# Performance work log

Measured on AMD Instinct MI355X. Metric: run time of the kernel, lower is better.

Reference implementation:

```python
import jax, jax.numpy as jnp
import numpy as np

B, S, D = 2, 2048, 1024
H, KVH, HD = 16, 1, 64
E, K, HID = 8, 2, 4096
EPS = 1e-5


def rmsnorm(x, scale):
    ms = jnp.mean(x * x, axis=-1, keepdims=True)
    return x * jax.lax.rsqrt(ms + EPS) * scale


def setup_inputs() -> dict:
    key = jax.random.key(0)
    ks = jax.random.split(key, 12)
    s = lambda k, shape, fan: jax.random.normal(k, shape, jnp.float32) * (fan ** -0.5)
    return {
        "x": jax.random.normal(ks[0], (B, S, D), jnp.float32),
        "g_pre_mqa": jnp.ones((D,), jnp.float32),
        "g_post_mqa": jnp.ones((D,), jnp.float32),
        "g_pre_moe": jnp.ones((D,), jnp.float32),
        "g_post_moe": jnp.ones((D,), jnp.float32),
        "Wq": s(ks[1], (D, H * HD), D),
        "Wk": s(ks[2], (D, KVH * HD), D),
        "Wv": s(ks[3], (D, KVH * HD), D),
        "Wo": s(ks[4], (H * HD, D), H * HD),
        "Wg": s(ks[5], (D, E), D),
        "We1": s(ks[6], (E, D, HID), D),
        "We2": s(ks[7], (E, HID, D), HID),
    }


def mqa(x, Wq, Wk, Wv, Wo):
    b, s, _ = x.shape
    q = (x @ Wq).reshape(b, s, H, HD).transpose(0, 2, 1, 3)     # [B,H,S,hd]
    k = (x @ Wk).reshape(b, s, KVH, HD).transpose(0, 2, 1, 3)   # [B,1,S,hd]
    v = (x @ Wv).reshape(b, s, KVH, HD).transpose(0, 2, 1, 3)
    scores = jnp.einsum('bhqd,bhkd->bhqk', q, jnp.broadcast_to(k, (b, H, s, HD))) / np.sqrt(HD)
    probs = jax.nn.softmax(scores, axis=-1)  # note: no causal mask, matching _standard_attention
    out = jnp.einsum('bhqk,bhkd->bhqd', probs, jnp.broadcast_to(v, (b, H, s, HD)))
    out = out.transpose(0, 2, 1, 3).reshape(b, s, H * HD)
    return out @ Wo


def moe(h, Wg, We1, We2):
    logits = h @ Wg                       # [B,S,E]
    probs = jax.nn.softmax(logits, axis=-1)
    topv, topi = jax.lax.top_k(probs, K)  # [B,S,K]
    # scatter top-k probs into full expert vector (non-chosen experts -> 0)
    routing = jnp.sum(jax.nn.one_hot(topi, E, dtype=h.dtype) * topv[..., None], axis=-2)  # [B,S,E]
    mid = jax.nn.gelu(jnp.einsum('bsd,edh->bseh', h, We1))
    eo = jnp.einsum('bseh,ehd->bsed', mid, We2)
    out = jnp.einsum('bse,bsed->bsd', routing, eo)
    return out, probs


def reference(x, g_pre_mqa, g_post_mqa, g_pre_moe, g_post_moe, Wq, Wk, Wv, Wo, Wg, We1, We2):
    # inference path: dropout and router noise disabled (training=False)
    x = x + rmsnorm(mqa(rmsnorm(x, g_pre_mqa), Wq, Wk, Wv, Wo), g_post_mqa)
    moe_out, routing_probs = moe(rmsnorm(x, g_pre_moe), Wg, We1, We2)
    x = x + rmsnorm(moe_out, g_post_moe)
    return x, routing_probs
```

## Files before the change

kernel.cpp:

```cpp
#include <hip/hip_runtime.h>
#include <hip/hip_bf16.h>
#include <math.h>

#define NTOK   4096
#define DMODEL 1024
#define SEQL   2048
#define QKVW   1152
#define NH     16
#define HDIM   64
#define NE     8
#define HIDD   4096
#define EPSV   1e-5f
#define KT     32

#define ASCL   256.f
#define WSCL   4096.f
#define OUTSCL (1.f/1048576.f)
#define SSCALE (0.125f/65536.f)
#define PBIAS  10.397207708399179f
#define DTHR   0.5f

typedef __attribute__((ext_vector_type(8))) short bf16x8;
typedef __attribute__((ext_vector_type(8))) _Float16 f16x8;
typedef __attribute__((ext_vector_type(4))) _Float16 f16x4;
typedef __attribute__((ext_vector_type(4))) float f32x4;

#define GLOBAL_AS __attribute__((address_space(1)))
#define LDS_AS    __attribute__((address_space(3)))
__device__ __forceinline__ void gl_lds16(const void* g, void* l){
  __builtin_amdgcn_global_load_lds((const GLOBAL_AS void*)g, (LDS_AS void*)l, 16u, 0, 0u);
}

__device__ __forceinline__ short f2b(float x){
  __hip_bfloat16 h = __float2bfloat16(x);
  return *reinterpret_cast<short*>(&h);
}
__device__ __forceinline__ void split2h(float x, _Float16& a, _Float16& b){
  a = (_Float16)x;
  b = (_Float16)(x - (float)a);
}

__global__ __launch_bounds__(256) void transpose_conv_kernel(
    const float* __restrict__ in, short* __restrict__ out,
    int R, int C, long inb, long outb)
{
  __shared__ float tile[32][33];
  in  += (size_t)blockIdx.z * inb;
  out += (size_t)blockIdx.z * outb;
  int c0 = blockIdx.x*32, r0 = blockIdx.y*32;
  int tx = threadIdx.x & 31, ty = threadIdx.x >> 5;
  #pragma unroll
  for (int i=0;i<4;i++)
    tile[ty+i*8][tx] = in[(size_t)(r0+ty+i*8)*C + c0+tx];
  __syncthreads();
  int cl = threadIdx.x >> 3, quad = threadIdx.x & 7;
  short4 s;
  s.x = f2b(tile[quad*4+0][cl]);
  s.y = f2b(tile[quad*4+1][cl]);
  s.z = f2b(tile[quad*4+2][cl]);
  s.w = f2b(tile[quad*4+3][cl]);
  *(short4*)&out[(size_t)(c0+cl)*R + r0 + quad*4] = s;
}

__global__ __launch_bounds__(256) void transpose_split2f16_kernel(
    const float* __restrict__ in, _Float16* __restrict__ o1, _Float16* __restrict__ o2,
    int R, int C, int rowOff, int outLD)
{
  __shared__ float tile[32][33];
  int c0 = blockIdx.x*32, r0 = blockIdx.y*32;
  int tx = threadIdx.x & 31, ty = threadIdx.x >> 5;
  #pragma unroll
  for (int i=0;i<4;i++)
    tile[ty+i*8][tx] = in[(size_t)(r0+ty+i*8)*C + c0+tx];
  __syncthreads();
  #pragma unroll
  for (int i=0;i<4;i++){
    float v = tile[tx][ty+i*8] * WSCL;
    _Float16 va,vb; split2h(v,va,vb);
    size_t idx = (size_t)(c0+ty+i*8+rowOff)*outLD + r0+tx;
    o1[idx]=va; o2[idx]=vb;
  }
}

__global__ __launch_bounds__(256) void rms_split2_kernel(
    const float* __restrict__ x, const float* __restrict__ g,
    _Float16* __restrict__ o1, _Float16* __restrict__ o2)
{
  int row = blockIdx.x, tid = threadIdx.x;
  const float4* xr = (const float4*)(x + (size_t)row*DMODEL);
  float4 v = xr[tid];
  float ss = v.x*v.x + v.y*v.y + v.z*v.z + v.w*v.w;
  #pragma unroll
  for (int off=32; off; off>>=1) ss += __shfl_down(ss, off);
  __shared__ float red[4];
  if ((tid&63)==0) red[tid>>6] = ss;
  __syncthreads();
  float rs = rsqrtf((red[0]+red[1]+red[2]+red[3])*(1.f/1024.f) + EPSV) * ASCL;
  float4 gv = ((const float4*)g)[tid];
  float o[4] = {v.x*rs*gv.x, v.y*rs*gv.y, v.z*rs*gv.z, v.w*rs*gv.w};
  f16x4 s1,s2;
  #pragma unroll
  for (int c=0;c<4;c++){ _Float16 a,b; split2h(o[c],a,b); s1[c]=a; s2[c]=b; }
  size_t base = (size_t)row*DMODEL + tid*4;
  *(f16x4*)(o1+base) = s1; *(f16x4*)(o2+base) = s2;
}

__global__ void split2_flat_kernel(const float* __restrict__ in,
    _Float16* __restrict__ o1, _Float16* __restrict__ o2, int n4)
{
  int i = blockIdx.x*256 + threadIdx.x;
  if (i >= n4) return;
  float4 v = ((const float4*)in)[i];
  float w[4] = {v.x*ASCL, v.y*ASCL, v.z*ASCL, v.w*ASCL};
  f16x4 s1,s2;
  #pragma unroll
  for (int c=0;c<4;c++){ _Float16 a,b; split2h(w[c],a,b); s1[c]=a; s2[c]=b; }
  ((f16x4*)o1)[i]=s1; ((f16x4*)o2)[i]=s2;
}

__global__ __launch_bounds__(256) void vtrans_split2_kernel(
    const float* __restrict__ qkv,
    _Float16* __restrict__ o1, _Float16* __restrict__ o2)
{
  __shared__ float tile[32][33];
  int s0 = blockIdx.x*32, d0 = blockIdx.y*32, bb = blockIdx.z;
  int tx = threadIdx.x & 31, ty = threadIdx.x >> 5;
  #pragma unroll
  for (int i=0;i<4;i++)
    tile[ty+i*8][tx] = qkv[(size_t)(bb*SEQL + s0+ty+i*8)*QKVW + DMODEL+HDIM + d0+tx];
  __syncthreads();
  #pragma unroll
  for (int i=0;i<4;i++){
    float v = tile[tx][ty+i*8] * ASCL;
    _Float16 va,vb; split2h(v,va,vb);
    size_t idx = (size_t)(bb*HDIM + d0+ty+i*8)*SEQL + s0+tx;
    o1[idx]=va; o2[idx]=vb;
  }
}

__global__ __launch_bounds__(256) void gemm_f16x2_kernel(
    const _Float16* __restrict__ a1, const _Float16* __restrict__ a2,
    const _Float16* __restrict__ b1, const _Float16* __restrict__ b2,
    float* __restrict__ C, int K, int ldc, float outscale)
{
  __shared__ _Float16 lsA[2][128*32];
  __shared__ _Float16 lsB[2][128*32];
  int m0 = blockIdx.y*128, n0 = blockIdx.x*128;
  int tid = threadIdx.x, wave = tid>>6, lane = tid&63;
  int g = lane>>4, li = lane&15;
  int wm = (wave>>1)*64, wn = (wave&1)*64;
  const _Float16* Ap[2] = {a1,a2};
  const _Float16* Bp[2] = {b1,b2};
  int srow = wave*32 + (lane>>2), scol = (lane&3)*8;
  const _Float16* gA[2][2]; const _Float16* gB[2][2];
  #pragma unroll
  for (int p=0;p<2;p++)
    #pragma unroll
    for (int i=0;i<2;i++){
      gA[p][i] = Ap[p] + (size_t)(m0+srow+i*16)*K + scol;
      gB[p][i] = Bp[p] + (size_t)(n0+srow+i*16)*K + scol;
    }
  f32x4 acc[4][4] = {};
  for (int k0=0; k0<K; k0+=32){
    #pragma unroll
    for (int p=0;p<2;p++)
      #pragma unroll
      for (int i=0;i<2;i++){
        gl_lds16(gA[p][i]+k0, &lsA[p][(wave*32+i*16)*32]);
        gl_lds16(gB[p][i]+k0, &lsB[p][(wave*32+i*16)*32]);
      }
    __syncthreads();
    #pragma unroll
    for (int i=0;i<2;i++){
      f16x8 af[4];
      #pragma unroll
      for (int m=0;m<4;m++) af[m] = *(f16x8*)&lsA[i][(wm+m*16+li)*32 + g*8];
      #pragma unroll
      for (int j=0;j<2-i;j++){
        #pragma unroll
        for (int n=0;n<4;n++){
          f16x8 bfr = *(f16x8*)&lsB[j][(wn+n*16+li)*32 + g*8];
          #pragma unroll
          for (int m=0;m<4;m++)
            acc[m][n] = __builtin_amdgcn_mfma_f32_16x16x32_f16(af[m], bfr, acc[m][n], 0,0,0);
        }
      }
    }
    __syncthreads();
  }
  #pragma unroll
  for (int m=0;m<4;m++){
    int lr0 = wm + m*16 + g*4;
    #pragma unroll
    for (int n=0;n<4;n++){
      int col = n0 + wn + n*16 + li;
      #pragma unroll
      for (int r=0;r<4;r++)
        C[(size_t)(m0+lr0+r)*ldc + col] = acc[m][n][r]*outscale;
    }
  }
}

__global__ __launch_bounds__(256) void attn_f16_kernel(
    const _Float16* __restrict__ q1, const _Float16* __restrict__ q2,
    const _Float16* __restrict__ v1, const _Float16* __restrict__ v2,
    _Float16* __restrict__ o1, _Float16* __restrict__ o2)
{
  __shared__ _Float16 Ks[32*136];
  __shared__ _Float16 Vs[64*72];
  int qt = blockIdx.x, h = blockIdx.y, b = blockIdx.z;
  int tid = threadIdx.x, wave = tid>>6, lane = tid&63;
  int g = lane>>4, li = lane&15;
  size_t qbase = (size_t)b*SEQL + qt*128;
  const _Float16* qsrc[2] = {q1,q2};
  const _Float16* vsrc[2] = {v1,v2};
  f16x8 qf[2][2][2];
  #pragma unroll
  for (int nf=0;nf<2;nf++){
    size_t qrow = qbase + wave*32 + nf*16 + li;
    #pragma unroll
    for (int j=0;j<2;j++)
      #pragma unroll
      for (int kk=0;kk<2;kk++)
        qf[nf][j][kk] = *(const f16x8*)(qsrc[j] + qrow*QKVW + h*HDIM + kk*32 + g*8);
  }
  float m_run[2] = {-1e30f,-1e30f}, l_run[2] = {0.f,0.f};
  f32x4 acc_o[4][2] = {};
  int src1 = (((2*g)&3)<<4) + li;
  int src2 = (((2*g+1)&3)<<4) + li;
  bool hi_half = (g>=2);

  for (int kvt=0; kvt<SEQL/KT; kvt++){
    __syncthreads();
    #pragma unroll
    for (int i=0;i<2;i++){
      int c = tid + 256*i;
      {
        int row = c>>4, sub = c&15;
        int pl = sub>>3, d = (sub&7)*8;
        *(f16x8*)&Ks[row*136 + pl*64 + d] =
          *(const f16x8*)(qsrc[pl] + ((size_t)b*SEQL + kvt*KT + row)*QKVW + DMODEL + d);
      }
      {
        int row = c>>3, sub = c&7;
        int pl = sub>>2, s8 = (sub&3)*8;
        *(f16x8*)&Vs[row*72 + pl*32 + s8] =
          *(const f16x8*)(vsrc[pl] + ((size_t)b*HDIM + row)*SEQL + kvt*KT + s8);
      }
    }
    __syncthreads();
    f32x4 s_acc[2][2] = {};
    #pragma unroll
    for (int i=0;i<2;i++){
      #pragma unroll
      for (int kk=0;kk<2;kk++){
        f16x8 af[2];
        #pragma unroll
        for (int mf=0;mf<2;mf++)
          af[mf] = *(f16x8*)&Ks[(mf*16+li)*136 + i*64 + kk*32 + g*8];
        #pragma unroll
        for (int j=0;j<2-i;j++){
          #pragma unroll
          for (int nf=0;nf<2;nf++){
            #pragma unroll
            for (int mf=0;mf<2;mf++)
              s_acc[mf][nf] = __builtin_amdgcn_mfma_f32_16x16x32_f16(af[mf], qf[nf][j][kk], s_acc[mf][nf], 0,0,0);
          }
        }
      }
    }
    float p[2][2][4];
    #pragma unroll
    for (int nf=0;nf<2;nf++){
      float mx = -1e30f;
      #pragma unroll
      for (int mf=0;mf<2;mf++)
        #pragma unroll
        for (int r=0;r<4;r++) mx = fmaxf(mx, s_acc[mf][nf][r]);
      mx = fmaxf(mx, __shfl_xor(mx,16));
      mx = fmaxf(mx, __shfl_xor(mx,32));
      mx *= SSCALE;
      if (!__all(mx <= m_run[nf] + DTHR)){
        float mn = fmaxf(m_run[nf], mx);
        float al = __expf(m_run[nf] - mn);
        m_run[nf] = mn;
        l_run[nf] *= al;
        #pragma unroll
        for (int mfd=0; mfd<4; mfd++){
          acc_o[mfd][nf][0]*=al; acc_o[mfd][nf][1]*=al;
          acc_o[mfd][nf][2]*=al; acc_o[mfd][nf][3]*=al;
        }
      }
      float rsum = 0.f;
      #pragma unroll
      for (int mf=0;mf<2;mf++)
        #pragma unroll
        for (int r=0;r<4;r++){
          float pv = __expf(s_acc[mf][nf][r]*SSCALE - m_run[nf] + PBIAS);
          p[mf][nf][r] = pv; rsum += pv;
        }
      rsum += __shfl_xor(rsum,16);
      rsum += __shfl_xor(rsum,32);
      l_run[nf] += rsum;
    }
    f16x8 fp_frag[2][2];
    #pragma unroll
    for (int nf=0;nf<2;nf++){
      float p8[8];
      #pragma unroll
      for (int jj=0;jj<4;jj++){
        float v0 = __shfl(p[0][nf][jj], src1);
        float vv1 = __shfl(p[1][nf][jj], src1);
        p8[jj] = hi_half ? vv1 : v0;
        float w0 = __shfl(p[0][nf][jj], src2);
        float w1 = __shfl(p[1][nf][jj], src2);
        p8[4+jj] = hi_half ? w1 : w0;
      }
      #pragma unroll
      for (int jj=0;jj<8;jj++){
        _Float16 xa,xb; split2h(p8[jj], xa,xb);
        fp_frag[nf][0][jj]=xa; fp_frag[nf][1][jj]=xb;
      }
    }
    #pragma unroll
    for (int vj=0;vj<2;vj++){
      f16x8 av[4];
      #pragma unroll
      for (int mfd=0;mfd<4;mfd++)
        av[mfd] = *(f16x8*)&Vs[(mfd*16+li)*72 + vj*32 + g*8];
      #pragma unroll
      for (int pi=0; pi<2-vj; pi++)
        #pragma unroll
        for (int mfd=0;mfd<4;mfd++)
          #pragma unroll
          for (int nf=0;nf<2;nf++)
            acc_o[mfd][nf] = __builtin_amdgcn_mfma_f32_16x16x32_f16(av[mfd], fp_frag[nf][pi], acc_o[mfd][nf], 0,0,0);
    }
  }
  #pragma unroll
  for (int nf=0;nf<2;nf++){
    float inv = 1.f/l_run[nf];
    size_t q = qbase + wave*32 + nf*16 + li;
    #pragma unroll
    for (int mfd=0;mfd<4;mfd++){
      int d0 = mfd*16 + g*4;
      f16x4 sa,sb;
      #pragma unroll
      for (int r=0;r<4;r++){
        _Float16 xa,xb; split2h(acc_o[mfd][nf][r]*inv, xa,xb);
        sa[r]=xa; sb[r]=xb;
      }
      size_t base = q*DMODEL + h*HDIM + d0;
      *(f16x4*)(o1+base)=sa; *(f16x4*)(o2+base)=sb;
    }
  }
}

__global__ __launch_bounds__(256) void attnres_kernel(
    const float* __restrict__ x, const float* __restrict__ ao,
    const float* __restrict__ gpost, const float* __restrict__ gpre,
    float* __restrict__ x2, short* __restrict__ h)
{
  int row = blockIdx.x, tid = threadIdx.x;
  float4 a  = ((const float4*)(ao + (size_t)row*DMODEL))[tid];
  float4 xv = ((const float4*)(x  + (size_t)row*DMODEL))[tid];
  float ss = a.x*a.x + a.y*a.y + a.z*a.z + a.w*a.w;
  #pragma unroll
  for (int off=32; off; off>>=1) ss += __shfl_down(ss, off);
  __shared__ float red[4];
  if ((tid&63)==0) red[tid>>6] = ss;
  __syncthreads();
  float rs1 = rsqrtf((red[0]+red[1]+red[2]+red[3])*(1.f/1024.f) + EPSV);
  float4 gp = ((const float4*)gpost)[tid];
  float4 o;
  o.x = xv.x + a.x*rs1*gp.x; o.y = xv.y + a.y*rs1*gp.y;
  o.z = xv.z + a.z*rs1*gp.z; o.w = xv.w + a.w*rs1*gp.w;
  ((float4*)(x2 + (size_t)row*DMODEL))[tid] = o;
  float s2 = o.x*o.x + o.y*o.y + o.z*o.z + o.w*o.w;
  __syncthreads();
  #pragma unroll
  for (int off=32; off; off>>=1) s2 += __shfl_down(s2, off);
  if ((tid&63)==0) red[tid>>6] = s2;
  __syncthreads();
  float rs2 = rsqrtf((red[0]+red[1]+red[2]+red[3])*(1.f/1024.f) + EPSV);
  float4 gm = ((const float4*)gpre)[tid];
  short4 hs;
  hs.x = f2b(o.x*rs2*gm.x); hs.y = f2b(o.y*rs2*gm.y);
  hs.z = f2b(o.z*rs2*gm.z); hs.w = f2b(o.w*rs2*gm.w);
  *(short4*)(h + (size_t)row*DMODEL + tid*4) = hs;
}

__global__ __launch_bounds__(64) void router_kernel(
    const float* __restrict__ x2, const float* __restrict__ g, const float* __restrict__ Wg,
    float* __restrict__ probs_out, int* __restrict__ tok_list, float* __restrict__ w_list,
    int* __restrict__ counts)
{
  int t = blockIdx.x, lane = threadIdx.x;
  const float4* xr = (const float4*)(x2 + (size_t)t*DMODEL);
  float4 v[4]; float ss = 0.f;
  #pragma unroll
  for (int i=0;i<4;i++){ v[i] = xr[lane + 64*i];
    ss += v[i].x*v[i].x + v[i].y*v[i].y + v[i].z*v[i].z + v[i].w*v[i].w; }
  #pragma unroll
  for (int off=32; off; off>>=1) ss += __shfl_xor(ss, off);
  float rs = rsqrtf(ss*(1.f/1024.f) + EPSV);
  float le[8] = {0,0,0,0,0,0,0,0};
  #pragma unroll
  for (int i=0;i<4;i++){
    int jb = (lane + 64*i)*4;
    float hv[4] = {v[i].x, v[i].y, v[i].z, v[i].w};
    #pragma unroll
    for (int c=0;c<4;c++){
      float hj = hv[c]*rs*g[jb+c];
      const float* wrow = Wg + (size_t)(jb+c)*NE;
      #pragma unroll
      for (int ee=0;ee<8;ee++) le[ee] += hj*wrow[ee];
    }
  }
  #pragma unroll
  for (int ee=0;ee<8;ee++)
    #pragma unroll
    for (int off=32; off; off>>=1) le[ee] += __shfl_xor(le[ee], off);
  float mx = le[0];
  #pragma unroll
  for (int ee=1;ee<8;ee++) mx = fmaxf(mx, le[ee]);
  float p[8], s = 0.f;
  #pragma unroll
  for (int ee=0;ee<8;ee++){ p[ee] = expf(le[ee]-mx); s += p[ee]; }
  float inv = 1.f/s;
  #pragma unroll
  for (int ee=0;ee<8;ee++) p[ee] *= inv;
  if (lane < 8) probs_out[(size_t)t*NE + lane] = p[lane];
  if (lane == 0){
    int i1 = 0;
    #pragma unroll
    for (int ee=1;ee<8;ee++) if (p[ee] > p[i1]) i1 = ee;
    int i2 = (i1==0) ? 1 : 0;
    #pragma unroll
    for (int ee=0;ee<8;ee++) if (ee != i1 && p[ee] > p[i2]) i2 = ee;
    int pos = atomicAdd(&counts[i1], 1);
    tok_list[i1*NTOK+pos] = t;
    w_list[i1*NTOK+pos] = p[i1];
    pos = atomicAdd(&counts[i2], 1);
    tok_list[i2*NTOK+pos] = t | (1<<16);
    w_list[i2*NTOK+pos] = p[i2];
  }
}

__global__ void prefix_kernel(const int* __restrict__ counts, int* __restrict__ bases){
  if (threadIdx.x == 0){
    int a = 0;
    for (int ee=0;ee<8;ee++){ bases[ee] = a; a += counts[ee]; }
  }
}

__global__ __launch_bounds__(256) void moe_gemm1_kernel(
    const short* __restrict__ h, const short* __restrict__ we1t,
    const int* __restrict__ tok_list, const int* __restrict__ counts,
    const int* __restrict__ bases, short* __restrict__ mid)
{
  int e = blockIdx.z;
  int cnt = counts[e];
  int m0 = blockIdx.y*128, n0 = blockIdx.x*128;
  if (m0 >= cnt) return;
  int base = bases[e];
  const short* Bt = we1t + (size_t)e*HIDD*DMODEL;
  const int* tl = tok_list + e*NTOK;
  __shared__ short lsA[128*32];
  __shared__ short lsB[128*32];
  int tid = threadIdx.x, wave = tid>>6, lane = tid&63;
  int li = lane&15, g = lane>>4;
  int wm = (wave>>1)*64, wn = (wave&1)*64;
  int srow = wave*32 + (lane>>2), scol = (lane&3)*8;
  const short* gA[2]; const short* gB[2];
  #pragma unroll
  for (int i=0;i<2;i++){
    int rr = min(m0+srow+i*16, cnt-1);
    gA[i] = h + (size_t)(tl[rr] & 0xFFFF)*DMODEL + scol;
    gB[i] = Bt + (size_t)(n0+srow+i*16)*DMODEL + scol;
  }
  f32x4 acc[4][4] = {};
  for (int k0=0; k0<DMODEL; k0+=32){
    #pragma unroll
    for (int i=0;i<2;i++){
      gl_lds16(gA[i]+k0, &lsA[(wave*32+i*16)*32]);
      gl_lds16(gB[i]+k0, &lsB[(wave*32+i*16)*32]);
    }
    __syncthreads();
    bf16x8 af[4], bfr[4];
    #pragma unroll
    for (int m=0;m<4;m++) af[m] = *(bf16x8*)&lsA[(wm+m*16+li)*32 + g*8];
    #pragma unroll
    for (int n=0;n<4;n++) bfr[n] = *(bf16x8*)&lsB[(wn+n*16+li)*32 + g*8];
    #pragma unroll
    for (int m=0;m<4;m++)
      #pragma unroll
      for (int n=0;n<4;n++)
        acc[m][n] = __builtin_amdgcn_mfma_f32_16x16x32_bf16(af[m], bfr[n], acc[m][n], 0,0,0);
    __syncthreads();
  }
  #pragma unroll
  for (int m=0;m<4;m++){
    int lr0 = wm + m*16 + (g<<2);
    #pragma unroll
    for (int n=0;n<4;n++){
      int col = n0 + wn + n*16 + li;
      #pragma unroll
      for (int r=0;r<4;r++){
        int gr = m0 + lr0 + r;
        if (gr < cnt){
          float tval = acc[m][n][r];
          float u = 1.5957691216057308f*(tval + 0.044715f*tval*tval*tval);
          float ge = tval / (1.f + __expf(-u));
          mid[(size_t)(base+gr)*HIDD + col] = f2b(ge);
        }
      }
    }
  }
}

__global__ __launch_bounds__(256) void moe_gemm2_kernel(
    const short* __restrict__ mid, const short* __restrict__ we2t,
    const int* __restrict__ tok_list, const float* __restrict__ w_list,
    const int* __restrict__ counts, const int* __restrict__ bases,
    float* __restrict__ eo)
{
  int e = blockIdx.z;
  int cnt = counts[e];
  int m0 = blockIdx.y*128, n0 = blockIdx.x*128;
  if (m0 >= cnt) return;
  int base = bases[e];
  const short* A  = mid + (size_t)base*HIDD;
  const short* Bt = we2t + (size_t)e*DMODEL*HIDD;
  const int* tl = tok_list + e*NTOK;
  const float* wl = w_list + e*NTOK;
  __shared__ short lsA[128*32];
  __shared__ short lsB[128*32];
  int tid = threadIdx.x, wave = tid>>6, lane = tid&63;
  int li = lane&15, g = lane>>4;
  int wm = (wave>>1)*64, wn = (wave&1)*64;
  int srow = wave*32 + (lane>>2), scol = (lane&3)*8;
  const short* gA[2]; const short* gB[2];
  #pragma unroll
  for (int i=0;i<2;i++){
    int rr = min(m0+srow+i*16, cnt-1);
    gA[i] = A + (size_t)rr*HIDD + scol;
    gB[i] = Bt + (size_t)(n0+srow+i*16)*HIDD + scol;
  }
  f32x4 acc[4][4] = {};
  for (int k0=0; k0<HIDD; k0+=32){
    #pragma unroll
    for (int i=0;i<2;i++){
      gl_lds16(gA[i]+k0, &lsA[(wave*32+i*16)*32]);
      gl_lds16(gB[i]+k0, &lsB[(wave*32+i*16)*32]);
    }
    __syncthreads();
    bf16x8 af[4], bfr[4];
    #pragma unroll
    for (int m=0;m<4;m++) af[m] = *(bf16x8*)&lsA[(wm+m*16+li)*32 + g*8];
    #pragma unroll
    for (int n=0;n<4;n++) bfr[n] = *(bf16x8*)&lsB[(wn+n*16+li)*32 + g*8];
    #pragma unroll
    for (int m=0;m<4;m++)
      #pragma unroll
      for (int n=0;n<4;n++)
        acc[m][n] = __builtin_amdgcn_mfma_f32_16x16x32_bf16(af[m], bfr[n], acc[m][n], 0,0,0);
    __syncthreads();
  }
  #pragma unroll
  for (int m=0;m<4;m++){
    int lr0 = wm + m*16 + (g<<2);
    #pragma unroll
    for (int n=0;n<4;n++){
      int col = n0 + wn + n*16 + li;
      #pragma unroll
      for (int r=0;r<4;r++){
        int gr = m0 + lr0 + r;
        if (gr < cnt){
          int pv = tl[gr];
          eo[((size_t)(pv>>16)*NTOK + (pv & 0xFFFF))*DMODEL + col] = wl[gr]*acc[m][n][r];
        }
      }
    }
  }
}

__global__ __launch_bounds__(256) void final_kernel(
    const float* __restrict__ x2, const float* __restrict__ eo,
    const float* __restrict__ g, float* __restrict__ out)
{
  int row = blockIdx.x, tid = threadIdx.x;
  float4 m0 = ((const float4*)(eo + (size_t)row*DMODEL))[tid];
  float4 m1 = ((const float4*)(eo + (size_t)(NTOK+row)*DMODEL))[tid];
  float4 mv;
  mv.x = m0.x+m1.x; mv.y = m0.y+m1.y; mv.z = m0.z+m1.z; mv.w = m0.w+m1.w;
  float4 xv = ((const float4*)(x2  + (size_t)row*DMODEL))[tid];
  float ss = mv.x*mv.x + mv.y*mv.y + mv.z*mv.z + mv.w*mv.w;
  #pragma unroll
  for (int off=32; off; off>>=1) ss += __shfl_down(ss, off);
  __shared__ float red[4];
  if ((tid&63)==0) red[tid>>6] = ss;
  __syncthreads();
  float rs = rsqrtf((red[0]+red[1]+red[2]+red[3])*(1.f/1024.f) + EPSV);
  float4 gv = ((const float4*)g)[tid];
  float4 o;
  o.x = xv.x + mv.x*rs*gv.x; o.y = xv.y + mv.y*rs*gv.y;
  o.z = xv.z + mv.z*rs*gv.z; o.w = xv.w + mv.w*rs*gv.w;
  ((float4*)(out + (size_t)row*DMODEL))[tid] = o;
}

extern "C" void kernel_launch(void* const* d_in, const int* in_sizes, int n_in,
                              void* d_out, int out_size, void* d_ws, size_t ws_size,
                              hipStream_t stream) {
  (void)in_sizes; (void)n_in; (void)out_size; (void)ws_size;
  const float* x          = (const float*)d_in[0];
  const float* g_pre_mqa  = (const float*)d_in[1];
  const float* g_post_mqa = (const float*)d_in[2];
  const float* g_pre_moe  = (const float*)d_in[3];
  const float* g_post_moe = (const float*)d_in[4];
  const float* Wq         = (const float*)d_in[5];
  const float* Wk         = (const float*)d_in[6];
  const float* Wv         = (const float*)d_in[7];
  const float* Wo         = (const float*)d_in[8];
  const float* Wg         = (const float*)d_in[9];
  const float* We1        = (const float*)d_in[10];
  const float* We2        = (const float*)d_in[11];

  float* out_x = (float*)d_out;
  float* out_probs = out_x + (size_t)NTOK*DMODEL;

  char* p = (char*)d_ws;
  size_t off = 0;
  auto alloc = [&](size_t bytes)->char*{
    char* r = p + off; off = (off + bytes + 255) & ~(size_t)255; return r; };

  short* we1t = (short*)alloc((size_t)NE*HIDD*DMODEL*2);
  short* we2t = (short*)alloc((size_t)NE*DMODEL*HIDD*2);
  short* mid  = (short*)alloc((size_t)2*NTOK*HIDD*2);

  char* regA = alloc((size_t)2*NTOK*DMODEL*2);
  _Float16* xn1p1 = (_Float16*)regA;
  _Float16* xn1p2 = (_Float16*)(regA + (size_t)NTOK*DMODEL*2);
  float* ao       = (float*)regA;

  _Float16* wqkvT1 = (_Float16*)alloc((size_t)QKVW*DMODEL*2);
  _Float16* wqkvT2 = (_Float16*)alloc((size_t)QKVW*DMODEL*2);
  _Float16* woT1   = (_Float16*)alloc((size_t)DMODEL*DMODEL*2);
  _Float16* woT2   = (_Float16*)alloc((size_t)DMODEL*DMODEL*2);

  char* regB = alloc((size_t)NTOK*QKVW*4);
  float* qkv = (float*)regB;
  _Float16* attnp1 = (_Float16*)regB;
  _Float16* attnp2 = (_Float16*)(regB + (size_t)NTOK*DMODEL*2);

  char* regC = alloc((size_t)2*NTOK*DMODEL*4 + (size_t)NTOK*DMODEL*2);
  _Float16* qkvf1 = (_Float16*)regC;
  _Float16* qkvf2 = (_Float16*)(regC + (size_t)NTOK*QKVW*2);
  float* eo    = (float*)regC;
  short* hbuf  = (short*)(regC + (size_t)2*NTOK*DMODEL*4);

  _Float16* vt1 = (_Float16*)alloc((size_t)2*HDIM*SEQL*2);
  _Float16* vt2 = (_Float16*)alloc((size_t)2*HDIM*SEQL*2);
  float* x2  = (float*)alloc((size_t)NTOK*DMODEL*4);
  int*   tok_l  = (int*)  alloc((size_t)NE*NTOK*4);
  float* w_l    = (float*)alloc((size_t)NE*NTOK*4);
  int*   counts = (int*)  alloc(256);
  int*   bases  = (int*)  alloc(256);

  transpose_conv_kernel<<<dim3(HIDD/32, DMODEL/32, NE), 256, 0, stream>>>(
      We1, we1t, DMODEL, HIDD, (long)DMODEL*HIDD, (long)HIDD*DMODEL);
  transpose_conv_kernel<<<dim3(DMODEL/32, HIDD/32, NE), 256, 0, stream>>>(
      We2, we2t, HIDD, DMODEL, (long)HIDD*DMODEL, (long)DMODEL*HIDD);
  transpose_split2f16_kernel<<<dim3(DMODEL/32, DMODEL/32), 256, 0, stream>>>(
      Wq, wqkvT1, wqkvT2, DMODEL, DMODEL, 0, DMODEL);
  transpose_split2f16_kernel<<<dim3(HDIM/32, DMODEL/32), 256, 0, stream>>>(
      Wk, wqkvT1, wqkvT2, DMODEL, HDIM, DMODEL, DMODEL);
  transpose_split2f16_kernel<<<dim3(HDIM/32, DMODEL/32), 256, 0, stream>>>(
      Wv, wqkvT1, wqkvT2, DMODEL, HDIM, DMODEL+HDIM, DMODEL);
  transpose_split2f16_kernel<<<dim3(DMODEL/32, DMODEL/32), 256, 0, stream>>>(
      Wo, woT1, woT2, DMODEL, DMODEL, 0, DMODEL);

  rms_split2_kernel<<<NTOK, 256, 0, stream>>>(x, g_pre_mqa, xn1p1, xn1p2);
  gemm_f16x2_kernel<<<dim3(QKVW/128, NTOK/128), 256, 0, stream>>>(
      xn1p1, xn1p2, wqkvT1, wqkvT2, qkv, DMODEL, QKVW, OUTSCL);
  split2_flat_kernel<<<(NTOK*QKVW/4 + 255)/256, 256, 0, stream>>>(
      qkv, qkvf1, qkvf2, NTOK*QKVW/4);
  vtrans_split2_kernel<<<dim3(SEQL/32, HDIM/32, 2), 256, 0, stream>>>(qkv, vt1, vt2);
  attn_f16_kernel<<<dim3(SEQL/128, NH, 2), 256, 0, stream>>>(
      qkvf1, qkvf2, vt1, vt2, attnp1, attnp2);
  gemm_f16x2_kernel<<<dim3(DMODEL/128, NTOK/128), 256, 0, stream>>>(
      attnp1, attnp2, woT1, woT2, ao, DMODEL, DMODEL, OUTSCL);
  attnres_kernel<<<NTOK, 256, 0, stream>>>(x, ao, g_post_mqa, g_pre_moe, x2, hbuf);

  hipMemsetAsync(counts, 0, 32, stream);
  router_kernel<<<NTOK, 64, 0, stream>>>(x2, g_pre_moe, Wg, out_probs, tok_l, w_l, counts);
  prefix_kernel<<<1, 64, 0, stream>>>(counts, bases);
  moe_gemm1_kernel<<<dim3(HIDD/128, NTOK/128, NE), 256, 0, stream>>>(
      hbuf, we1t, tok_l, counts, bases, mid);
  moe_gemm2_kernel<<<dim3(DMODEL/128, NTOK/128, NE), 256, 0, stream>>>(
      mid, we2t, tok_l, w_l, counts, bases, eo);
  final_kernel<<<NTOK, 256, 0, stream>>>(x2, eo, g_post_moe, out_x);
}
```

Measured before the change: 771.9 us.

## Fuse QKV split into GEMM epilogue and prefetch K/V tiles in attention

The QKV GEMM now writes the two-way f16 split directly in its epilogue, which removes the fp32 qkv buffer and the separate split2_flat pass. The V-transpose kernel now reads and recombines the split halves instead of the fp32 buffer. The attention kernel prefetches the next K/V tile into registers while the current one is being computed, and raises wave priority around the MFMA sections with s_setprio. The trade-off is higher register pressure in attention and scattered 2-byte stores in the GEMM epilogue.

```diff
diff --git a/kernel.cpp b/kernel.cpp
--- a/kernel.cpp
+++ b/kernel.cpp
@@ -105,33 +105,22 @@
   *(f16x4*)(o1+base) = s1; *(f16x4*)(o2+base) = s2;
 }
 
-__global__ void split2_flat_kernel(const float* __restrict__ in,
-    _Float16* __restrict__ o1, _Float16* __restrict__ o2, int n4)
-{
-  int i = blockIdx.x*256 + threadIdx.x;
-  if (i >= n4) return;
-  float4 v = ((const float4*)in)[i];
-  float w[4] = {v.x*ASCL, v.y*ASCL, v.z*ASCL, v.w*ASCL};
-  f16x4 s1,s2;
-  #pragma unroll
-  for (int c=0;c<4;c++){ _Float16 a,b; split2h(w[c],a,b); s1[c]=a; s2[c]=b; }
-  ((f16x4*)o1)[i]=s1; ((f16x4*)o2)[i]=s2;
-}
-
 __global__ __launch_bounds__(256) void vtrans_split2_kernel(
-    const float* __restrict__ qkv,
+    const _Float16* __restrict__ p1, const _Float16* __restrict__ p2,
     _Float16* __restrict__ o1, _Float16* __restrict__ o2)
 {
   __shared__ float tile[32][33];
   int s0 = blockIdx.x*32, d0 = blockIdx.y*32, bb = blockIdx.z;
   int tx = threadIdx.x & 31, ty = threadIdx.x >> 5;
   #pragma unroll
-  for (int i=0;i<4;i++)
-    tile[ty+i*8][tx] = qkv[(size_t)(bb*SEQL + s0+ty+i*8)*QKVW + DMODEL+HDIM + d0+tx];
+  for (int i=0;i<4;i++){
+    size_t idx = (size_t)(bb*SEQL + s0+ty+i*8)*QKVW + DMODEL+HDIM + d0+tx;
+    tile[ty+i*8][tx] = (float)p1[idx] + (float)p2[idx];
+  }
   __syncthreads();
   #pragma unroll
   for (int i=0;i<4;i++){
-    float v = tile[tx][ty+i*8] * ASCL;
+    float v = tile[tx][ty+i*8];
     _Float16 va,vb; split2h(v,va,vb);
     size_t idx = (size_t)(bb*HDIM + d0+ty+i*8)*SEQL + s0+tx;
     o1[idx]=va; o2[idx]=vb;
@@ -201,6 +190,73 @@
   }
 }
 
+__global__ __launch_bounds__(256) void gemm_f16x2s_kernel(
+    const _Float16* __restrict__ a1, const _Float16* __restrict__ a2,
+    const _Float16* __restrict__ b1, const _Float16* __restrict__ b2,
+    _Float16* __restrict__ o1, _Float16* __restrict__ o2, int K, int ldc, float outscale)
+{
+  __shared__ _Float16 lsA[2][128*32];
+  __shared__ _Float16 lsB[2][128*32];
+  int m0 = blockIdx.y*128, n0 = blockIdx.x*128;
+  int tid = threadIdx.x, wave = tid>>6, lane = tid&63;
+  int g = lane>>4, li = lane&15;
+  int wm = (wave>>1)*64, wn = (wave&1)*64;
+  const _Float16* Ap[2] = {a1,a2};
+  const _Float16* Bp[2] = {b1,b2};
+  int srow = wave*32 + (lane>>2), scol = (lane&3)*8;
+  const _Float16* gA[2][2]; const _Float16* gB[2][2];
+  #pragma unroll
+  for (int p=0;p<2;p++)
+    #pragma unroll
+    for (int i=0;i<2;i++){
+      gA[p][i] = Ap[p] + (size_t)(m0+srow+i*16)*K + scol;
+      gB[p][i] = Bp[p] + (size_t)(n0+srow+i*16)*K + scol;
+    }
+  f32x4 acc[4][4] = {};
+  for (int k0=0; k0<K; k0+=32){
+    #pragma unroll
+    for (int p=0;p<2;p++)
+      #pragma unroll
+      for (int i=0;i<2;i++){
+        gl_lds16(gA[p][i]+k0, &lsA[p][(wave*32+i*16)*32]);
+        gl_lds16(gB[p][i]+k0, &lsB[p][(wave*32+i*16)*32]);
+      }
+    __syncthreads();
+    #pragma unroll
+    for (int i=0;i<2;i++){
+      f16x8 af[4];
+      #pragma unroll
+      for (int m=0;m<4;m++) af[m] = *(f16x8*)&lsA[i][(wm+m*16+li)*32 + g*8];
+      #pragma unroll
+      for (int j=0;j<2-i;j++){
+        #pragma unroll
+        for (int n=0;n<4;n++){
+          f16x8 bfr = *(f16x8*)&lsB[j][(wn+n*16+li)*32 + g*8];
+          #pragma unroll
+          for (int m=0;m<4;m++)
+            acc[m][n] = __builtin_amdgcn_mfma_f32_16x16x32_f16(af[m], bfr, acc[m][n], 0,0,0);
+        }
+      }
+    }
+    __syncthreads();
+  }
+  #pragma unroll
+  for (int m=0;m<4;m++){
+    int lr0 = wm + m*16 + g*4;
+    #pragma unroll
+    for (int n=0;n<4;n++){
+      int col = n0 + wn + n*16 + li;
+      #pragma unroll
+      for (int r=0;r<4;r++){
+        float val = acc[m][n][r]*outscale;
+        _Float16 xa,xb; split2h(val,xa,xb);
+        size_t idx = (size_t)(m0+lr0+r)*ldc + col;
+        o1[idx]=xa; o2[idx]=xb;
+      }
+    }
+  }
+}
+
 __global__ __launch_bounds__(256) void attn_f16_kernel(
     const _Float16* __restrict__ q1, const _Float16* __restrict__ q2,
     const _Float16* __restrict__ v1, const _Float16* __restrict__ v2,
@@ -224,6 +280,22 @@
       for (int kk=0;kk<2;kk++)
         qf[nf][j][kk] = *(const f16x8*)(qsrc[j] + qrow*QKVW + h*HDIM + kk*32 + g*8);
   }
+  const _Float16* kga[2]; int klds[2];
+  const _Float16* vga[2]; int vlds[2];
+  #pragma unroll
+  for (int i=0;i<2;i++){
+    int c = tid + 256*i;
+    { int row=c>>4, sub=c&15, pl=sub>>3, d=(sub&7)*8;
+      kga[i] = qsrc[pl] + ((size_t)b*SEQL + row)*QKVW + DMODEL + d;
+      klds[i] = row*136 + pl*64 + d; }
+    { int row=c>>3, sub=c&7, pl=sub>>2, s8=(sub&3)*8;
+      vga[i] = vsrc[pl] + ((size_t)b*HDIM + row)*SEQL + s8;
+      vlds[i] = row*72 + pl*32 + s8; }
+  }
+  f16x8 kreg[2], vreg[2];
+  #pragma unroll
+  for (int i=0;i<2;i++){ kreg[i]=*(const f16x8*)kga[i]; vreg[i]=*(const f16x8*)vga[i]; }
+
   float m_run[2] = {-1e30f,-1e30f}, l_run[2] = {0.f,0.f};
   f32x4 acc_o[4][2] = {};
   int src1 = (((2*g)&3)<<4) + li;
@@ -231,25 +303,21 @@
   bool hi_half = (g>=2);
 
   for (int kvt=0; kvt<SEQL/KT; kvt++){
-    __syncthreads();
     #pragma unroll
     for (int i=0;i<2;i++){
-      int c = tid + 256*i;
-      {
-        int row = c>>4, sub = c&15;
-        int pl = sub>>3, d = (sub&7)*8;
-        *(f16x8*)&Ks[row*136 + pl*64 + d] =
-          *(const f16x8*)(qsrc[pl] + ((size_t)b*SEQL + kvt*KT + row)*QKVW + DMODEL + d);
-      }
-      {
-        int row = c>>3, sub = c&7;
-        int pl = sub>>2, s8 = (sub&3)*8;
-        *(f16x8*)&Vs[row*72 + pl*32 + s8] =
-          *(const f16x8*)(vsrc[pl] + ((size_t)b*HDIM + row)*SEQL + kvt*KT + s8);
-      }
-    }
-    __syncthreads();
+      *(f16x8*)&Ks[klds[i]] = kreg[i];
+      *(f16x8*)&Vs[vlds[i]] = vreg[i];
+    }
+    __syncthreads();
+    if (kvt+1 < SEQL/KT){
+      #pragma unroll
+      for (int i=0;i<2;i++){
+        kreg[i] = *(const f16x8*)(kga[i] + (size_t)(kvt+1)*KT*QKVW);
+        vreg[i] = *(const f16x8*)(vga[i] + (size_t)(kvt+1)*KT);
+      }
+    }
     f32x4 s_acc[2][2] = {};
+    __builtin_amdgcn_s_setprio(1);
     #pragma unroll
     for (int i=0;i<2;i++){
       #pragma unroll
@@ -269,6 +337,7 @@
         }
       }
     }
+    __builtin_amdgcn_s_setprio(0);
     float p[2][2][4];
     #pragma unroll
     for (int nf=0;nf<2;nf++){
@@ -322,6 +391,7 @@
         fp_frag[nf][0][jj]=xa; fp_frag[nf][1][jj]=xb;
       }
     }
+    __builtin_amdgcn_s_setprio(1);
     #pragma unroll
     for (int vj=0;vj<2;vj++){
       f16x8 av[4];
@@ -336,6 +406,8 @@
           for (int nf=0;nf<2;nf++)
             acc_o[mfd][nf] = __builtin_amdgcn_mfma_f32_16x16x32_f16(av[mfd], fp_frag[nf][pi], acc_o[mfd][nf], 0,0,0);
     }
+    __builtin_amdgcn_s_setprio(0);
+    __syncthreads();
   }
   #pragma unroll
   for (int nf=0;nf<2;nf++){
@@ -648,8 +720,7 @@
   _Float16* woT1   = (_Float16*)alloc((size_t)DMODEL*DMODEL*2);
   _Float16* woT2   = (_Float16*)alloc((size_t)DMODEL*DMODEL*2);
 
-  char* regB = alloc((size_t)NTOK*QKVW*4);
-  float* qkv = (float*)regB;
+  char* regB = alloc((size_t)2*NTOK*DMODEL*2);
   _Float16* attnp1 = (_Float16*)regB;
   _Float16* attnp2 = (_Float16*)(regB + (size_t)NTOK*DMODEL*2);
 
@@ -681,11 +752,9 @@
       Wo, woT1, woT2, DMODEL, DMODEL, 0, DMODEL);
 
   rms_split2_kernel<<<NTOK, 256, 0, stream>>>(x, g_pre_mqa, xn1p1, xn1p2);
-  gemm_f16x2_kernel<<<dim3(QKVW/128, NTOK/128), 256, 0, stream>>>(
-      xn1p1, xn1p2, wqkvT1, wqkvT2, qkv, DMODEL, QKVW, OUTSCL);
-  split2_flat_kernel<<<(NTOK*QKVW/4 + 255)/256, 256, 0, stream>>>(
-      qkv, qkvf1, qkvf2, NTOK*QKVW/4);
-  vtrans_split2_kernel<<<dim3(SEQL/32, HDIM/32, 2), 256, 0, stream>>>(qkv, vt1, vt2);
+  gemm_f16x2s_kernel<<<dim3(QKVW/128, NTOK/128), 256, 0, stream>>>(
+      xn1p1, xn1p2, wqkvT1, wqkvT2, qkvf1, qkvf2, DMODEL, QKVW, OUTSCL*ASCL);
+  vtrans_split2_kernel<<<dim3(SEQL/32, HDIM/32, 2), 256, 0, stream>>>(qkvf1, qkvf2, vt1, vt2);
   attn_f16_kernel<<<dim3(SEQL/128, NH, 2), 256, 0, stream>>>(
       qkvf1, qkvf2, vt1, vt2, attnp1, attnp2);
   gemm_f16x2_kernel<<<dim3(DMODEL/128, NTOK/128), 256, 0, stream>>>(
```

Measured after the change: 745.5 us. -3.4%, faster.
